# Kernel optimization log

Hardware: AMD Instinct MI355X
Metric: run time of the kernel (lower is better)

The kernel has to match this reference:

```python
import jax, jax.numpy as jnp
import numpy as np

EPS_BN = 1e-5


def conv2d(x, w, b=None, pad=0, groups=1):
    y = jax.lax.conv_general_dilated(
        x, w, window_strides=(1, 1), padding=[(pad, pad), (pad, pad)],
        dimension_numbers=('NCHW', 'OIHW', 'NCHW'), feature_group_count=groups)
    if b is not None:
        y = y + b[None, :, None, None]
    return y


def bilinear_sample(x, py, px):
    # x: (C,H,W); py,px: (T,Ho,Wo) fractional sample coords. Zero outside borders
    # (matches torchvision deform_conv2d per-corner masking).
    C, H, W = x.shape
    xf = x.reshape(C, -1)
    y0 = jnp.floor(py)
    x0 = jnp.floor(px)

    def g(yi, xi):
        valid = (yi >= 0) & (yi <= H - 1) & (xi >= 0) & (xi <= W - 1)
        idx = (jnp.clip(yi, 0, H - 1).astype(jnp.int32) * W
               + jnp.clip(xi, 0, W - 1).astype(jnp.int32))
        v = xf[:, idx.reshape(-1)].reshape((C,) + idx.shape)  # (C,T,Ho,Wo)
        return jnp.where(valid[None], v, 0.0)

    wy1 = py - y0
    wx1 = px - x0
    wy0 = 1.0 - wy1
    wx0 = 1.0 - wx1
    return (g(y0, x0) * (wy0 * wx0)[None]
            + g(y0, x0 + 1.0) * (wy0 * wx1)[None]
            + g(y0 + 1.0, x0) * (wy1 * wx0)[None]
            + g(y0 + 1.0, x0 + 1.0) * (wy1 * wx1)[None])


def deform_depthwise(x, offset, dyn_w, k):
    # x: (B,C,H,W); offset: (B,2*k*k,H,W) interleaved (dy,dx) per tap;
    # dyn_w: (B,C,k,k) per-sample depthwise kernels. stride=1, pad=k//2.
    B, C, H, W = x.shape
    T = k * k
    pad = k // 2
    off = offset.reshape(B, T, 2, H, W)
    ky, kx = jnp.meshgrid(jnp.arange(k), jnp.arange(k), indexing='ij')
    base_y = (jnp.arange(H)[None, :, None] - pad
              + ky.reshape(T)[:, None, None]).astype(x.dtype)  # (T,H,1)
    base_x = (jnp.arange(W)[None, None, :] - pad
              + kx.reshape(T)[:, None, None]).astype(x.dtype)  # (T,1,W)
    py = base_y[None] + off[:, :, 0]  # (B,T,H,W)
    px = base_x[None] + off[:, :, 1]
    v = jax.vmap(bilinear_sample)(x, py, px)  # (B,C,T,H,W)
    return jnp.einsum('bct,bcthw->bchw', dyn_w.reshape(B, C, T), v)


def reference(F_c, dec_w, dec_b, off1_w, off1_b, off2_w, off2_b,
              akg_dw_w, akg_head_w, akg_head_b, pw2_w, pw2_b,
              bn_gamma, bn_beta):
    k = 3
    Kd = 7
    B, C, H, W = F_c.shape
    R = dec_w.shape[0]

    # TargetRegionDecoupler: F_i = F * M_i + F
    M = jax.nn.softmax(conv2d(F_c, dec_w, dec_b), axis=1)  # (B,R,H,W)

    outs = []
    for i in range(R):
        F_i = F_c * (1.0 + M[:, i:i + 1])
        # OffsetGenerator
        h = jax.nn.relu(conv2d(F_i, off1_w[i], off1_b[i], pad=1))
        p_i = conv2d(h, off2_w[i], off2_b[i], pad=1)  # (B,2*k*k,H,W)
        # AdaptiveKernelGenerator (exact adaptive pool: 56 -> 7 via 8x8 mean)
        d = F_i.reshape(B, C, Kd, H // Kd, Kd, W // Kd).mean(axis=(3, 5))
        d = jax.nn.relu(conv2d(d, akg_dw_w[i], None, pad=1, groups=C))
        d = d.mean(axis=(2, 3), keepdims=True)  # AdaptiveAvgPool2d(1)
        K_i = jnp.tanh(conv2d(d, akg_head_w[i], akg_head_b[i]).reshape(B, C, k, k))
        # per-sample dynamic depthwise deformable conv
        outs.append(deform_depthwise(F_i, p_i, K_i, k))

    O = conv2d(jnp.concatenate(outs, axis=1), pw2_w, pw2_b)
    # BatchNorm2d, training-mode batch statistics
    mean = O.mean(axis=(0, 2, 3), keepdims=True)
    var = O.var(axis=(0, 2, 3), keepdims=True)
    O = (O - mean) * jax.lax.rsqrt(var + EPS_BN)
    O = O * bn_gamma[None, :, None, None] + bn_beta[None, :, None, None]
    return O


def setup_inputs() -> dict:
    key = jax.random.key(0)
    ks = jax.random.split(key, 10)
    B, C, H, W = 8, 256, 56, 56
    k, R = 3, 2
    hid = max(32, C // 4)
    return {
        'F_c': jax.random.normal(ks[0], (B, C, H, W), jnp.float32),
        'dec_w': jax.random.normal(ks[1], (R, C, 1, 1), jnp.float32) * 0.1,
        'dec_b': jnp.zeros((R,), jnp.float32),
        'off1_w': jax.random.normal(ks[2], (R, hid, C, 3, 3), jnp.float32) * 0.05,
        'off1_b': jnp.zeros((R, hid), jnp.float32),
        'off2_w': jax.random.normal(ks[3], (R, 2 * k * k, hid, 3, 3), jnp.float32) * 0.01,
        'off2_b': jnp.zeros((R, 2 * k * k), jnp.float32),
        'akg_dw_w': jax.random.normal(ks[4], (R, C, 1, 3, 3), jnp.float32) * 0.1,
        'akg_head_w': jax.random.normal(ks[5], (R, C * k * k, C, 1, 1), jnp.float32) * 0.05,
        'akg_head_b': jnp.zeros((R, C * k * k), jnp.float32),
        'pw2_w': jax.random.normal(ks[6], (C, R * C, 1, 1), jnp.float32) * 0.05,
        'pw2_b': jnp.zeros((C,), jnp.float32),
        'bn_gamma': jnp.ones((C,), jnp.float32),
        'bn_beta': jnp.zeros((C,), jnp.float32),
    }
```

## Files before the change

kernel.cpp:

```cpp
#include <hip/hip_runtime.h>
#include <hip/hip_bf16.h>

#define BB 8
#define CC_ 256
#define HH 56
#define WW 56
#define HWSZ (HH*WW)
#define RR_ 2
#define HID 64
#define FPR ((size_t)8*58*58*256)
#define HPR ((size_t)8*58*58*64)
#define NPIX ((size_t)BB*HWSZ)

typedef __hip_bfloat16 bf16;
typedef __attribute__((ext_vector_type(8))) short short8;
typedef __attribute__((ext_vector_type(4))) short short4_t;
typedef __attribute__((ext_vector_type(4))) float f32x4;

struct Tap { int o00, o01, o10, o11; float w00, w01, w10, w11; };

__device__ __forceinline__ float b2f(bf16 v){ return __bfloat162float(v); }
__device__ __forceinline__ bf16 f2b(float v){ return __float2bfloat16(v); }
__device__ __forceinline__ float bs2f(short s){ return __uint_as_float(((unsigned)(unsigned short)s)<<16); }

__global__ __launch_bounds__(256) void k_scalepack(const float* __restrict__ F, const float* __restrict__ dec_w,
                                                   const float* __restrict__ dec_b,
                                                   bf16* __restrict__ Fp, float* __restrict__ rowsum){
    __shared__ float lds_f[256][57];
    __shared__ float lw0[256], lw1[256];
    __shared__ float ls0[56], ls1[56];
    int bx = blockIdx.x; int b = bx/HH, gy = bx%HH;
    int tid = threadIdx.x;
    lw0[tid] = dec_w[tid]; lw1[tid] = dec_w[CC_+tid];
    const float* Fb = F + (size_t)b*CC_*HWSZ + gy*WW;
    for (int it = 0; it < 56; ++it){
        int idx = it*256 + tid;
        int c = idx / 56, x = idx - c*56;
        lds_f[c][x] = Fb[(size_t)c*HWSZ + x];
    }
    __syncthreads();
    if (tid < 56){
        float a0 = dec_b[0], a1 = dec_b[1];
        for (int c = 0; c < CC_; ++c){ float v = lds_f[c][tid]; a0 += v*lw0[c]; a1 += v*lw1[c]; }
        float m = fmaxf(a0,a1);
        float e0 = __expf(a0-m), e1 = __expf(a1-m);
        float inv = 1.0f/(e0+e1);
        ls0[tid] = 1.0f + e0*inv; ls1[tid] = 1.0f + e1*inv;
    }
    __syncthreads();
    bf16 z = f2b(0.f);
    for (int r = 0; r < 2; ++r){
        const float* lsr = r ? ls1 : ls0;
        bf16* slab = Fp + (size_t)r*FPR + (size_t)b*58*58*256;
        bf16* dst = slab + ((size_t)(gy+1)*58 + 1)*256 + tid;
        for (int x2 = 0; x2 < 56; ++x2) dst[(size_t)x2*256] = f2b(lds_f[tid][x2] * lsr[x2]);
        float* rs = rowsum + ((((size_t)(r*8+b)*56 + gy)*7))*256 + tid;
        #pragma unroll
        for (int v = 0; v < 7; ++v){
            float sum = 0.f;
            #pragma unroll
            for (int k = 0; k < 8; ++k) sum += lds_f[tid][v*8+k] * lsr[v*8+k];
            rs[(size_t)v*256] = sum;
        }
        bf16* rowp = slab + (size_t)(gy+1)*58*256;
        rowp[tid] = z;
        rowp[57*256 + tid] = z;
        if (gy == 0){ for (int cidx = 0; cidx < 58; ++cidx) slab[(size_t)cidx*256 + tid] = z; }
        if (gy == 55){ bf16* r57 = slab + (size_t)57*58*256;
                       for (int cidx = 0; cidx < 58; ++cidx) r57[(size_t)cidx*256 + tid] = z; }
    }
}

__global__ void k_bprep_all(const float* __restrict__ w1, const float* __restrict__ wpw,
                            const float* __restrict__ wc2,
                            bf16* __restrict__ Bp, bf16* __restrict__ Bpw, bf16* __restrict__ Bc){
    int id = blockIdx.x;
    int L = threadIdx.x;
    if (id < 576){
        int nt = id & 3; id >>= 2; int icc = id & 7; id >>= 3; int t = id % 9; int r = id / 9;
        int oc = nt*16 + (L&15);
        const float* wr = w1 + (size_t)r*HID*CC_*9;
        bf16* out = Bp + (((((size_t)r*9 + t)*8 + icc)*4 + nt)*64 + L)*8;
        #pragma unroll
        for (int j = 0; j < 8; ++j){
            int ic = icc*32 + (L>>4)*8 + j;
            out[j] = f2b(wr[((size_t)oc*CC_ + ic)*9 + t]);
        }
    } else if (id < 832){
        id -= 576;
        int kk = id >> 4, nt = id & 15;
        int oc = nt*16 + (L&15);
        bf16* out = Bpw + (((size_t)(kk*16+nt))*64 + L)*8;
        #pragma unroll
        for (int j = 0; j < 8; ++j){
            int ic = kk*32 + (L>>4)*8 + j;
            out[j] = f2b(wpw[(size_t)oc*512 + ic]);
        }
    } else {
        id -= 832;
        int nt = id & 1; id >>= 1; int ks = id % 18; int r = id / 18;
        int t = ks >> 1, chunk = ks & 1;
        int oc = nt*16 + (L&15);
        const float* wr = wc2 + (size_t)r*18*HID*9;
        bf16* out = Bc + ((((size_t)r*18 + ks)*2 + nt)*64 + L)*8;
        #pragma unroll
        for (int j = 0; j < 8; ++j){
            int ic = chunk*32 + (L>>4)*8 + j;
            out[j] = (oc < 18) ? f2b(wr[((size_t)oc*HID + ic)*9 + t]) : f2b(0.f);
        }
    }
}

__global__ __launch_bounds__(256) void k_conv1(const bf16* __restrict__ Fp, const bf16* __restrict__ Bp,
                                               const float* __restrict__ bias, bf16* __restrict__ hp){
    int bx = blockIdx.x; int b = bx & 7; int rid = bx >> 3; int yp = rid % 28; int r = rid / 28;
    int y0 = yp*2;
    int tid = threadIdx.x; int wave = tid>>6, lane = tid&63;
    int m = lane&15, q = lane>>4;
    int x0 = (wave==3) ? 40 : wave*16;
    f32x4 acc[2][4];
    #pragma unroll
    for (int i=0;i<2;++i)
        #pragma unroll
        for (int j=0;j<4;++j) acc[i][j] = (f32x4){0,0,0,0};
    const bf16* Fb = Fp + (size_t)r*FPR + ((size_t)b*58*58)*256;
    const bf16* Bpr = Bp + (size_t)r*9*8*4*64*8;
    #pragma unroll
    for (int t = 0; t < 9; ++t){
        int ty = t/3, tx = t%3;
        const bf16* arow = Fb + ((size_t)(y0+ty)*58 + (x0+m+tx))*256 + q*8;
        const bf16* brow = Bpr + ((size_t)t*8)*4*64*8 + lane*8;
        #pragma unroll
        for (int icc = 0; icc < 8; ++icc){
            short8 a0 = *(const short8*)(arow + icc*32);
            short8 a1 = *(const short8*)(arow + 58*256 + icc*32);
            const bf16* bb = brow + (size_t)icc*4*64*8;
            short8 b0 = *(const short8*)(bb);
            short8 b1 = *(const short8*)(bb + 64*8);
            short8 b2 = *(const short8*)(bb + 2*64*8);
            short8 b3 = *(const short8*)(bb + 3*64*8);
            acc[0][0] = __builtin_amdgcn_mfma_f32_16x16x32_bf16(a0, b0, acc[0][0], 0, 0, 0);
            acc[1][0] = __builtin_amdgcn_mfma_f32_16x16x32_bf16(a1, b0, acc[1][0], 0, 0, 0);
            acc[0][1] = __builtin_amdgcn_mfma_f32_16x16x32_bf16(a0, b1, acc[0][1], 0, 0, 0);
            acc[1][1] = __builtin_amdgcn_mfma_f32_16x16x32_bf16(a1, b1, acc[1][1], 0, 0, 0);
            acc[0][2] = __builtin_amdgcn_mfma_f32_16x16x32_bf16(a0, b2, acc[0][2], 0, 0, 0);
            acc[1][2] = __builtin_amdgcn_mfma_f32_16x16x32_bf16(a1, b2, acc[1][2], 0, 0, 0);
            acc[0][3] = __builtin_amdgcn_mfma_f32_16x16x32_bf16(a0, b3, acc[0][3], 0, 0, 0);
            acc[1][3] = __builtin_amdgcn_mfma_f32_16x16x32_bf16(a1, b3, acc[1][3], 0, 0, 0);
        }
    }
    const float* br = bias + r*HID;
    bf16* slab = hp + (size_t)r*HPR + (size_t)b*58*58*64;
    bf16 z = f2b(0.f);
    #pragma unroll
    for (int rr = 0; rr < 2; ++rr){
        int y = y0 + rr;
        bf16* hrow = slab + ((size_t)(y+1)*58 + 1)*64;
        #pragma unroll
        for (int nt = 0; nt < 4; ++nt){
            int oc = nt*16 + m;
            float bv = br[oc];
            #pragma unroll
            for (int r2 = 0; r2 < 4; ++r2){
                int x = x0 + q*4 + r2;
                hrow[(size_t)x*64 + oc] = f2b(fmaxf(acc[rr][nt][r2] + bv, 0.f));
            }
        }
        bf16* rowp = slab + (size_t)(y+1)*58*64;
        if (tid < 64) rowp[tid] = z;
        else if (tid < 128) rowp[57*64 + (tid-64)] = z;
        if (y == 0){ for (int idx = tid; idx < 58*64; idx += 256) slab[idx] = z; }
        if (y == 55){ bf16* r57 = slab + (size_t)57*58*64;
                      for (int idx = tid; idx < 58*64; idx += 256) r57[idx] = z; }
    }
}

__global__ __launch_bounds__(256) void k_conv2m(const bf16* __restrict__ hp, const bf16* __restrict__ Bc,
                                                const float* __restrict__ bias, Tap* __restrict__ tap){
    __shared__ float pld[18][56];
    int bx = blockIdx.x; int b = bx & 7; int rid = bx >> 3; int y = rid % 56; int r = rid / 56;
    int tid = threadIdx.x; int wave = tid>>6, lane = tid&63;
    int m = lane&15, q = lane>>4;
    int x0 = (wave==3) ? 40 : wave*16;
    f32x4 acc0 = {0,0,0,0}, acc1 = {0,0,0,0};
    const bf16* Hb = hp + (size_t)r*HPR + ((size_t)b*58 + y)*58*64;
    const bf16* Bcr = Bc + (size_t)r*18*2*64*8;
    #pragma unroll
    for (int t = 0; t < 9; ++t){
        int ty = t/3, tx = t%3;
        const bf16* arow = Hb + ((size_t)ty*58 + (x0+m+tx))*64 + q*8;
        #pragma unroll
        for (int chunk = 0; chunk < 2; ++chunk){
            short8 a = *(const short8*)(arow + chunk*32);
            const bf16* bb = Bcr + (((size_t)(t*2+chunk))*2*64 + lane)*8;
            short8 b0 = *(const short8*)(bb);
            short8 b1 = *(const short8*)(bb + 64*8);
            acc0 = __builtin_amdgcn_mfma_f32_16x16x32_bf16(a, b0, acc0, 0, 0, 0);
            acc1 = __builtin_amdgcn_mfma_f32_16x16x32_bf16(a, b1, acc1, 0, 0, 0);
        }
    }
    const float* br = bias + r*18;
    #pragma unroll
    for (int r2 = 0; r2 < 4; ++r2){
        int x = x0 + q*4 + r2;
        pld[m][x] = acc0[r2] + br[m];
        if (m < 2) pld[16+m][x] = acc1[r2] + br[16+m];
    }
    __syncthreads();
    for (int e = tid; e < 504; e += 256){
        int t = e / 56, x = e % 56;
        int ky = t / 3, kx = t % 3;
        float dy = pld[2*t][x];
        float dx = pld[2*t+1][x];
        float py = (float)(y - 1 + ky) + dy;
        float px = (float)(x - 1 + kx) + dx;
        float y0f = floorf(py), x0f = floorf(px);
        float wy1 = py - y0f, wx1 = px - x0f;
        float wy0 = 1.f - wy1, wx0 = 1.f - wx1;
        float vy0 = (y0f >= 0.f  && y0f <= 55.f) ? 1.f : 0.f;
        float vy1 = (y0f >= -1.f && y0f <= 54.f) ? 1.f : 0.f;
        float vx0 = (x0f >= 0.f  && x0f <= 55.f) ? 1.f : 0.f;
        float vx1 = (x0f >= -1.f && x0f <= 54.f) ? 1.f : 0.f;
        int yy0 = (int)y0f, x0i = (int)x0f;
        int iy0 = min(max(yy0,0),55),   iy1 = min(max(yy0+1,0),55);
        int ix0 = min(max(x0i,0),55),   ix1 = min(max(x0i+1,0),55);
        Tap td;
        td.o00 = ((iy0+1)*58 + ix0+1)*256;
        td.o01 = ((iy0+1)*58 + ix1+1)*256;
        td.o10 = ((iy1+1)*58 + ix0+1)*256;
        td.o11 = ((iy1+1)*58 + ix1+1)*256;
        td.w00 = wy0*wx0*vy0*vx0;
        td.w01 = wy0*wx1*vy0*vx1;
        td.w10 = wy1*wx0*vy1*vx0;
        td.w11 = wy1*wx1*vy1*vx1;
        size_t pid = ((size_t)(r*8 + b))*3136 + y*56 + x;
        tap[pid*9 + t] = td;
    }
}

__global__ __launch_bounds__(256) void k_akg_s(const float* __restrict__ rowsum, const float* __restrict__ dw,
                                               float* __restrict__ s){
    int rb = blockIdx.x; int r = rb >> 3;
    int c = threadIdx.x;
    const float* rs = rowsum + ((size_t)rb*56*7)*256 + c;
    float d[7][7];
    #pragma unroll
    for (int u = 0; u < 7; ++u)
        #pragma unroll
        for (int v = 0; v < 7; ++v){
            float acc = 0.f;
            #pragma unroll
            for (int k = 0; k < 8; ++k) acc += rs[(size_t)((u*8+k)*7 + v)*256];
            d[u][v] = acc * (1.f/64.f);
        }
    const float* wp = dw + (size_t)r*CC_*9 + c*9;
    float w[9];
    #pragma unroll
    for (int k = 0; k < 9; ++k) w[k] = wp[k];
    float tot = 0.f;
    #pragma unroll
    for (int u = 0; u < 7; ++u)
        #pragma unroll
        for (int v = 0; v < 7; ++v){
            float acc = 0.f;
            #pragma unroll
            for (int ky = 0; ky < 3; ++ky){
                int uu = u+ky-1; if ((unsigned)uu >= 7u) continue;
                #pragma unroll
                for (int kx = 0; kx < 3; ++kx){
                    int vv = v+kx-1; if ((unsigned)vv >= 7u) continue;
                    acc += d[uu][vv]*w[ky*3+kx];
                }
            }
            tot += fmaxf(acc, 0.f);
        }
    s[(size_t)rb*CC_ + c] = tot * (1.f/49.f);
}

__global__ void k_akg_head(const float* __restrict__ s, const float* __restrict__ hw,
                           const float* __restrict__ hb, float* __restrict__ Kw){
    int gid = blockIdx.x; int r = gid / 72; int id = gid % 72;
    int b = id / 9; int og = id % 9;
    __shared__ float sv[CC_];
    int tid = threadIdx.x;
    sv[tid] = s[(size_t)(r*8+b)*CC_ + tid];
    __syncthreads();
    int o = og*256 + tid;
    const float* wp = hw + (size_t)r*2304*CC_ + (size_t)o*CC_;
    float acc = hb[(size_t)r*2304 + o];
    for (int c2=0;c2<CC_;++c2) acc += wp[c2]*sv[c2];
    int c = o / 9, t = o - 9*c;
    Kw[((size_t)r*BB + b)*2304 + t*256 + c] = tanhf(acc);
}

__global__ __launch_bounds__(256, 8) void k_deform(const bf16* __restrict__ Fp, const Tap* __restrict__ tap,
                                                   const float* __restrict__ Kw, bf16* __restrict__ outsN){
    __shared__ float klds[2304];
    int bx = blockIdx.x; int b = bx & 7; int rest = bx >> 3;
    int pg = rest % 392; int creg = rest / 392;
    int tid = threadIdx.x; int w = tid >> 6, l = tid & 63;
    int wu = __builtin_amdgcn_readfirstlane(w);
    int yx0 = pg*8 + wu*2;
    size_t slab = (size_t)(creg*8 + b)*3136;
    const float* Kb = Kw + ((size_t)creg*8 + b)*2304;
    for (int i = tid*4; i < 2304; i += 1024) *(f32x4*)&klds[i] = *(const f32x4*)(Kb + i);
    __syncthreads();
    int h = l >> 5, li = l & 31;
    const Tap* tdp = tap + (slab + yx0 + h)*9;
    const bf16* Fb = Fp + (size_t)creg*FPR + (size_t)b*58*58*256;
    int c0 = li*8;
    float acc[8];
    #pragma unroll
    for (int j = 0; j < 8; ++j) acc[j] = 0.f;
    #pragma unroll 3
    for (int t = 0; t < 9; ++t){
        Tap d = tdp[t];
        short8 f00 = *(const short8*)(Fb + d.o00 + c0);
        short8 f01 = *(const short8*)(Fb + d.o01 + c0);
        short8 f10 = *(const short8*)(Fb + d.o10 + c0);
        short8 f11 = *(const short8*)(Fb + d.o11 + c0);
        f32x4 klo = *(const f32x4*)&klds[t*256 + c0];
        f32x4 khi = *(const f32x4*)&klds[t*256 + c0 + 4];
        #pragma unroll
        for (int j = 0; j < 4; ++j){
            float v = d.w00*bs2f(f00[j]) + d.w01*bs2f(f01[j]) + d.w10*bs2f(f10[j]) + d.w11*bs2f(f11[j]);
            acc[j] += klo[j]*v;
        }
        #pragma unroll
        for (int j = 4; j < 8; ++j){
            float v = d.w00*bs2f(f00[j]) + d.w01*bs2f(f01[j]) + d.w10*bs2f(f10[j]) + d.w11*bs2f(f11[j]);
            acc[j] += khi[j-4]*v;
        }
    }
    __attribute__((aligned(16))) bf16 tmp[8];
    #pragma unroll
    for (int j = 0; j < 8; ++j) tmp[j] = f2b(acc[j]);
    *(short8*)(outsN + ((size_t)b*HWSZ + yx0 + h)*512 + creg*256 + c0) = *(const short8*)tmp;
}

__global__ __launch_bounds__(256) void k_pw2_mstats(const bf16* __restrict__ outsN, const bf16* __restrict__ Bpw,
                                                    const float* __restrict__ bias, float* __restrict__ stats,
                                                    float* __restrict__ O){
    __shared__ float ls[2][2][256];
    int tid = threadIdx.x; int wave = tid>>6, lane = tid&63;
    int pixGroup = wave>>1, ntH = wave&1;
    int m = lane&15, q = lane>>4;
    size_t pb = (size_t)blockIdx.x*64 + pixGroup*32;
    const bf16* Ap0 = outsN + (pb + m)*512 + q*8;
    const bf16* Ap1 = Ap0 + (size_t)16*512;
    f32x4 acc[2][8];
    #pragma unroll
    for (int g=0;g<2;++g)
        #pragma unroll
        for (int i=0;i<8;++i) acc[g][i] = (f32x4){0,0,0,0};
    #pragma unroll 1
    for (int kk = 0; kk < 16; ++kk){
        short8 a0 = *(const short8*)(Ap0 + kk*32);
        short8 a1 = *(const short8*)(Ap1 + kk*32);
        const bf16* Bk = Bpw + (((size_t)kk*16 + ntH*8)*64 + lane)*8;
        #pragma unroll
        for (int nt2 = 0; nt2 < 8; ++nt2){
            short8 b = *(const short8*)(Bk + (size_t)nt2*64*8);
            acc[0][nt2] = __builtin_amdgcn_mfma_f32_16x16x32_bf16(a0, b, acc[0][nt2], 0, 0, 0);
            acc[1][nt2] = __builtin_amdgcn_mfma_f32_16x16x32_bf16(a1, b, acc[1][nt2], 0, 0, 0);
        }
    }
    #pragma unroll
    for (int nt2 = 0; nt2 < 8; ++nt2){
        int oc = ntH*128 + nt2*16 + m;
        float bv = bias[oc];
        float s1 = 0.f, s2 = 0.f;
        #pragma unroll
        for (int g = 0; g < 2; ++g){
            size_t pbg = pb + g*16;
            int b_idx = (int)(pbg / HWSZ);
            int yx0 = (int)(pbg % HWSZ);
            float* op = O + ((size_t)b_idx*CC_ + oc)*HWSZ + yx0 + q*4;
            #pragma unroll
            for (int r = 0; r < 4; ++r){
                float v = acc[g][nt2][r] + bv;
                op[r] = v;
                s1 += v; s2 += v*v;
            }
        }
        s1 += __shfl_down(s1, 32); s1 += __shfl_down(s1, 16);
        s2 += __shfl_down(s2, 32); s2 += __shfl_down(s2, 16);
        if (q == 0){ ls[pixGroup][0][oc] = s1; ls[pixGroup][1][oc] = s2; }
    }
    __syncthreads();
    if (tid < 256){
        atomicAdd(&stats[tid],       ls[0][0][tid] + ls[1][0][tid]);
        atomicAdd(&stats[256 + tid], ls[0][1][tid] + ls[1][1][tid]);
    }
}

__global__ __launch_bounds__(256) void k_bnapply(const float* __restrict__ O, const float* __restrict__ stats,
                                                 const float* __restrict__ gamma, const float* __restrict__ beta,
                                                 float* __restrict__ out){
    int n = (blockIdx.x*256 + threadIdx.x)*4;
    int c = (n / HWSZ) % CC_;
    float ninv = 1.f/(float)NPIX;
    float mean = stats[c]*ninv;
    float var = fmaxf(stats[256+c]*ninv - mean*mean, 0.f);
    float rsq = rsqrtf(var + 1e-5f);
    float g = gamma[c], be = beta[c];
    f32x4 v = *(const f32x4*)(O + n);
    f32x4 o;
    #pragma unroll
    for (int j = 0; j < 4; ++j) o[j] = (v[j] - mean)*rsq*g + be;
    *(f32x4*)(out + n) = o;
}

extern "C" void kernel_launch(void* const* d_in, const int* in_sizes, int n_in,
                              void* d_out, int out_size, void* d_ws, size_t ws_size,
                              hipStream_t stream) {
    (void)in_sizes; (void)n_in; (void)out_size; (void)ws_size;
    const float* F_c    = (const float*)d_in[0];
    const float* dec_w  = (const float*)d_in[1];
    const float* dec_b  = (const float*)d_in[2];
    const float* off1_w = (const float*)d_in[3];
    const float* off1_b = (const float*)d_in[4];
    const float* off2_w = (const float*)d_in[5];
    const float* off2_b = (const float*)d_in[6];
    const float* akg_dw = (const float*)d_in[7];
    const float* akg_hw = (const float*)d_in[8];
    const float* akg_hb = (const float*)d_in[9];
    const float* pw2_w  = (const float*)d_in[10];
    const float* pw2_b  = (const float*)d_in[11];
    const float* gamma  = (const float*)d_in[12];
    const float* beta   = (const float*)d_in[13];
    float* out = (float*)d_out;

    char* ws = (char*)d_ws;
    size_t off = 0;
    auto alloc = [&](size_t bytes)->char*{
        char* r = ws + off;
        off = (off + bytes + 255) & ~(size_t)255;
        return r;
    };
    bf16*  Fp    = (bf16*) alloc(2*FPR*2);
    bf16*  Bp    = (bf16*) alloc((size_t)2*9*8*4*64*8*2);
    bf16*  Bpw   = (bf16*) alloc((size_t)16*16*64*8*2);
    bf16*  Bc    = (bf16*) alloc((size_t)2*18*2*64*8*2);
    float* rowsum= (float*)alloc((size_t)2*8*56*7*256*4);
    bf16*  hp    = (bf16*) alloc(2*HPR*2);
    float* s     = (float*)alloc((size_t)2*BB*CC_*4);
    float* Kw    = (float*)alloc((size_t)2*BB*CC_*9*4);
    bf16*  outsN = (bf16*) alloc(NPIX*512*2);
    Tap*   tap   = (Tap*)  alloc((size_t)2*NPIX*9*sizeof(Tap));
    float* stats = (float*)alloc(2*CC_*4);
    float* O = (float*)Fp;

    hipMemsetAsync(stats, 0, 2*CC_*sizeof(float), stream);

    k_scalepack<<<dim3(BB*HH), dim3(256), 0, stream>>>(F_c, dec_w, dec_b, Fp, rowsum);
    k_bprep_all<<<dim3(904), dim3(64), 0, stream>>>(off1_w, pw2_w, off2_w, Bp, Bpw, Bc);

    k_conv1<<<dim3(2*BB*28), dim3(256), 0, stream>>>(Fp, Bp, off1_b, hp);
    k_conv2m<<<dim3(2*BB*HH), dim3(256), 0, stream>>>(hp, Bc, off2_b, tap);
    k_akg_s<<<dim3(16), dim3(256), 0, stream>>>(rowsum, akg_dw, s);
    k_akg_head<<<dim3(2*BB*9), dim3(256), 0, stream>>>(s, akg_hw, akg_hb, Kw);
    k_deform<<<dim3(2*BB*392), dim3(256), 0, stream>>>(Fp, tap, Kw, outsN);

    k_pw2_mstats<<<dim3(392), dim3(256), 0, stream>>>(outsN, Bpw, pw2_b, stats, O);
    k_bnapply<<<dim3((int)(NPIX*CC_/1024)), dim3(256), 0, stream>>>(O, stats, gamma, beta, out);
}
```

Before: 288.4 us.

## Split conv1 input-channel reduction across two wave groups with LDS reduction

```diff
diff --git a/kernel.cpp b/kernel.cpp
--- a/kernel.cpp
+++ b/kernel.cpp
@@ -111,13 +111,15 @@
     }
 }
 
-__global__ __launch_bounds__(256) void k_conv1(const bf16* __restrict__ Fp, const bf16* __restrict__ Bp,
-                                               const float* __restrict__ bias, bf16* __restrict__ hp){
+__global__ __launch_bounds__(512, 4) void k_conv1(const bf16* __restrict__ Fp, const bf16* __restrict__ Bp,
+                                                  const float* __restrict__ bias, bf16* __restrict__ hp){
+    __shared__ float red[4][64][36];
     int bx = blockIdx.x; int b = bx & 7; int rid = bx >> 3; int yp = rid % 28; int r = rid / 28;
     int y0 = yp*2;
     int tid = threadIdx.x; int wave = tid>>6, lane = tid&63;
     int m = lane&15, q = lane>>4;
-    int x0 = (wave==3) ? 40 : wave*16;
+    int xq = wave & 3, kh = wave >> 2;
+    int x0 = (xq==3) ? 40 : xq*16;
     f32x4 acc[2][4];
     #pragma unroll
     for (int i=0;i<2;++i)
@@ -128,13 +130,13 @@
     #pragma unroll
     for (int t = 0; t < 9; ++t){
         int ty = t/3, tx = t%3;
-        const bf16* arow = Fb + ((size_t)(y0+ty)*58 + (x0+m+tx))*256 + q*8;
-        const bf16* brow = Bpr + ((size_t)t*8)*4*64*8 + lane*8;
-        #pragma unroll
-        for (int icc = 0; icc < 8; ++icc){
-            short8 a0 = *(const short8*)(arow + icc*32);
-            short8 a1 = *(const short8*)(arow + 58*256 + icc*32);
-            const bf16* bb = brow + (size_t)icc*4*64*8;
+        const bf16* arow = Fb + ((size_t)(y0+ty)*58 + (x0+m+tx))*256 + q*8 + kh*128;
+        const bf16* brow = Bpr + ((size_t)(t*8 + kh*4))*4*64*8 + lane*8;
+        #pragma unroll
+        for (int i = 0; i < 4; ++i){
+            short8 a0 = *(const short8*)(arow + i*32);
+            short8 a1 = *(const short8*)(arow + 58*256 + i*32);
+            const bf16* bb = brow + (size_t)i*4*64*8;
             short8 b0 = *(const short8*)(bb);
             short8 b1 = *(const short8*)(bb + 64*8);
             short8 b2 = *(const short8*)(bb + 2*64*8);
@@ -149,29 +151,47 @@
             acc[1][3] = __builtin_amdgcn_mfma_f32_16x16x32_bf16(a1, b3, acc[1][3], 0, 0, 0);
         }
     }
+    if (kh){
+        #pragma unroll
+        for (int rr = 0; rr < 2; ++rr)
+            #pragma unroll
+            for (int nt = 0; nt < 4; ++nt)
+                #pragma unroll
+                for (int j = 0; j < 4; ++j)
+                    red[xq][lane][rr*16 + nt*4 + j] = acc[rr][nt][j];
+    }
+    __syncthreads();
     const float* br = bias + r*HID;
     bf16* slab = hp + (size_t)r*HPR + (size_t)b*58*58*64;
     bf16 z = f2b(0.f);
+    if (!kh){
+        const float* rp = &red[xq][lane][0];
+        #pragma unroll
+        for (int rr = 0; rr < 2; ++rr){
+            int y = y0 + rr;
+            bf16* hrow = slab + ((size_t)(y+1)*58 + 1)*64;
+            #pragma unroll
+            for (int nt = 0; nt < 4; ++nt){
+                int oc = nt*16 + m;
+                float bv = br[oc];
+                #pragma unroll
+                for (int r2 = 0; r2 < 4; ++r2){
+                    int x = x0 + q*4 + r2;
+                    float v = acc[rr][nt][r2] + rp[rr*16 + nt*4 + r2];
+                    hrow[(size_t)x*64 + oc] = f2b(fmaxf(v + bv, 0.f));
+                }
+            }
+        }
+    }
     #pragma unroll
     for (int rr = 0; rr < 2; ++rr){
         int y = y0 + rr;
-        bf16* hrow = slab + ((size_t)(y+1)*58 + 1)*64;
-        #pragma unroll
-        for (int nt = 0; nt < 4; ++nt){
-            int oc = nt*16 + m;
-            float bv = br[oc];
-            #pragma unroll
-            for (int r2 = 0; r2 < 4; ++r2){
-                int x = x0 + q*4 + r2;
-                hrow[(size_t)x*64 + oc] = f2b(fmaxf(acc[rr][nt][r2] + bv, 0.f));
-            }
-        }
         bf16* rowp = slab + (size_t)(y+1)*58*64;
         if (tid < 64) rowp[tid] = z;
         else if (tid < 128) rowp[57*64 + (tid-64)] = z;
-        if (y == 0){ for (int idx = tid; idx < 58*64; idx += 256) slab[idx] = z; }
+        if (y == 0){ for (int idx = tid; idx < 58*64; idx += 512) slab[idx] = z; }
         if (y == 55){ bf16* r57 = slab + (size_t)57*58*64;
-                      for (int idx = tid; idx < 58*64; idx += 256) r57[idx] = z; }
+                      for (int idx = tid; idx < 58*64; idx += 512) r57[idx] = z; }
     }
 }
 
@@ -456,7 +476,7 @@
     k_scalepack<<<dim3(BB*HH), dim3(256), 0, stream>>>(F_c, dec_w, dec_b, Fp, rowsum);
     k_bprep_all<<<dim3(904), dim3(64), 0, stream>>>(off1_w, pw2_w, off2_w, Bp, Bpw, Bc);
 
-    k_conv1<<<dim3(2*BB*28), dim3(256), 0, stream>>>(Fp, Bp, off1_b, hp);
+    k_conv1<<<dim3(2*BB*28), dim3(512), 0, stream>>>(Fp, Bp, off1_b, hp);
     k_conv2m<<<dim3(2*BB*HH), dim3(256), 0, stream>>>(hp, Bc, off2_b, tap);
     k_akg_s<<<dim3(16), dim3(256), 0, stream>>>(rowsum, akg_dw, s);
     k_akg_head<<<dim3(2*BB*9), dim3(256), 0, stream>>>(s, akg_hw, akg_hb, Kw);
```

After: 288.0 us. No clear change (-0.1%).
